# Kernel optimization log

Hardware: AMD Instinct MI355X
Metric: run time of the kernel (lower is better)

## Reference

```python
import jax, jax.numpy as jnp
import numpy as np

BS, D_IN, D_OUT, N_MASKS = 1024, 512, 512, 8

def setup_inputs() -> dict:
    key = jax.random.key(0)
    k1, k2, k3, k4 = jax.random.split(key, 4)
    x = jax.random.normal(k1, (BS, D_IN), dtype=jnp.float32)
    state = jax.random.randint(k2, (BS,), 0, N_MASKS, dtype=jnp.int32)
    # glorot-uniform-like kernel
    limit = float(np.sqrt(6.0 / (D_IN + D_OUT)))
    kernel = jax.random.uniform(k3, (D_IN, D_OUT), dtype=jnp.float32, minval=-limit, maxval=limit)
    # binary MADE connectivity masks (0/1)
    masks = (jax.random.uniform(k4, (N_MASKS, D_IN, D_OUT)) < 0.5).astype(jnp.float32)
    return {"x": x, "state": state, "kernel": kernel, "masks": masks}

def reference(x, state, kernel, masks):
    # Math of original: out = relu(x[b] @ (kernel * masks[state[b]]))
    # Efficient form: precompute all n masked kernels (small n), batched matmul,
    # then gather per-sample result. Avoids materializing [bs, d_in, d_out].
    masked = kernel[None, :, :] * masks            # [n, d_in, d_out]
    y_all = jnp.einsum('bi,nio->bno', x, masked)   # [bs, n, d_out]
    y = jnp.take_along_axis(y_all, state[:, None, None].astype(jnp.int32), axis=1)[:, 0, :]
    return jax.nn.relu(y)
```

## Files before the change

### kernel.cpp

```cpp
#include <hip/hip_runtime.h>

#define BS 1024
#define D_IN 512
#define D_OUT 512
#define N_MASKS 8

typedef short bf16x8 __attribute__((ext_vector_type(8)));
typedef float f32x4 __attribute__((ext_vector_type(4)));

#define WF_OFF_USH (8192 / 2)
#define WF_USH     (N_MASKS * 16 * 32 * 512)
#define XB_OFF_USH (WF_OFF_USH + WF_USH)

__device__ __forceinline__ ushort f2bf(float f) {
    union { float f; unsigned u; } x; x.f = f;
    unsigned r = (x.u + 0x7fffu + ((x.u >> 16) & 1u)) >> 16;
    return (ushort)r;
}

__global__ void __launch_bounds__(256) prep_kernel(
    const float* __restrict__ x, const int* __restrict__ state,
    const float* __restrict__ kern, const float* __restrict__ masks,
    int* __restrict__ wsi, ushort* __restrict__ wf, ushort* __restrict__ xb)
{
    __shared__ float prod[32][133];
    const int bx  = blockIdx.x;
    const int tid = threadIdx.x;

    if (bx < 512) {
        const int n  = bx >> 6;
        const int kb = (bx >> 2) & 15;
        const int cg = bx & 3;
        const int k0 = kb * 32, c0 = cg * 128;
        const float* maskn = masks + (size_t)n * (D_IN * D_OUT);

        #pragma unroll
        for (int it = 0; it < 4; ++it) {
            const int i  = it * 256 + tid;
            const int r  = i >> 5;
            const int c4 = i & 31;
            const size_t gidx = (size_t)(k0 + r) * D_OUT + c0 + c4 * 4;
            const float4 kv = *(const float4*)&kern[gidx];
            const float4 mv = *(const float4*)&maskn[gidx];
            float* dst = &prod[r][c4 * 4];
            dst[0] = kv.x * mv.x; dst[1] = kv.y * mv.y;
            dst[2] = kv.z * mv.z; dst[3] = kv.w * mv.w;
        }
        __syncthreads();

        #pragma unroll
        for (int it = 0; it < 2; ++it) {
            const int c = it * 64 + (tid >> 2);
            const int q = tid & 3;
            uint pk[4];
            #pragma unroll
            for (int h = 0; h < 4; ++h) {
                const float v0 = prod[q * 8 + 2 * h][c];
                const float v1 = prod[q * 8 + 2 * h + 1][c];
                pk[h] = (uint)f2bf(v0) | ((uint)f2bf(v1) << 16);
            }
            uint4 o; o.x = pk[0]; o.y = pk[1]; o.z = pk[2]; o.w = pk[3];
            const int cb = cg * 8 + (c >> 4);
            const int l  = q * 16 + (c & 15);
            *(uint4*)(wf + ((size_t)((n * 16 + kb) * 32 + cb)) * 512 + l * 8) = o;
        }
    } else if (bx < 768) {
        const int idx = (bx - 512) * 256 + tid;
        const float4 a = ((const float4*)x)[idx * 2];
        const float4 b = ((const float4*)x)[idx * 2 + 1];
        uint4 o;
        o.x = (uint)f2bf(a.x) | ((uint)f2bf(a.y) << 16);
        o.y = (uint)f2bf(a.z) | ((uint)f2bf(a.w) << 16);
        o.z = (uint)f2bf(b.x) | ((uint)f2bf(b.y) << 16);
        o.w = (uint)f2bf(b.z) | ((uint)f2bf(b.w) << 16);
        *(uint4*)(xb + (size_t)idx * 8) = o;
    } else {
        __shared__ int cnt[N_MASKS];
        __shared__ int offs[N_MASKS + 1];
        if (tid < N_MASKS) cnt[tid] = 0;
        __syncthreads();
        int s[4];
        #pragma unroll
        for (int r = 0; r < 4; ++r) {
            s[r] = state[r * 256 + tid];
            atomicAdd(&cnt[s[r]], 1);
        }
        __syncthreads();
        if (tid == 0) {
            int acc = 0;
            for (int i = 0; i < N_MASKS; ++i) { offs[i] = acc; acc += cnt[i]; }
            offs[N_MASKS] = acc;
        }
        __syncthreads();
        if (tid <= N_MASKS) wsi[tid] = offs[tid];
        if (tid < N_MASKS) cnt[tid] = offs[tid];
        __syncthreads();
        #pragma unroll
        for (int r = 0; r < 4; ++r) {
            const int pos = atomicAdd(&cnt[s[r]], 1);
            wsi[16 + pos] = r * 256 + tid;
        }
    }
}

__global__ void __launch_bounds__(256, 4) gemm_kernel(
    const ushort* __restrict__ xb, const ushort* __restrict__ wf,
    const int* __restrict__ wsi, float* __restrict__ out)
{
    const int n   = blockIdx.x;
    const int cb0 = blockIdx.y * 2;
    const int off0 = wsi[n];
    const int off1 = wsi[n + 1];
    const int gcnt = off1 - off0;

    const int tid  = threadIdx.x;
    const int lane = tid & 63;
    const int wid  = tid >> 6;
    const int g    = lane >> 4;
    const int cl   = lane & 15;

    __shared__ float red[3][2][64][4];

    const ushort* wp0 = wf + ((size_t)((n * 16 + wid * 4) * 32 + cb0)) * 512 + lane * 8;

    for (int rt = blockIdx.z; rt * 16 < gcnt; rt += 8) {
        const int p  = off0 + rt * 16 + cl;
        const int rv = (p < off1) ? wsi[16 + p] : -1;
        const ushort* xr = xb + (size_t)(rv < 0 ? 0 : rv) * D_IN + wid * 4 * 32 + g * 8;

        f32x4 acc0 = {0.f, 0.f, 0.f, 0.f};
        f32x4 acc1 = {0.f, 0.f, 0.f, 0.f};
        #pragma unroll
        for (int i = 0; i < 4; ++i) {
            const bf16x8 a  = *(const bf16x8*)(xr + i * 32);
            const bf16x8 b0 = *(const bf16x8*)(wp0 + (size_t)i * 32 * 512);
            const bf16x8 b1 = *(const bf16x8*)(wp0 + (size_t)i * 32 * 512 + 512);
            acc0 = __builtin_amdgcn_mfma_f32_16x16x32_bf16(a, b0, acc0, 0, 0, 0);
            acc1 = __builtin_amdgcn_mfma_f32_16x16x32_bf16(a, b1, acc1, 0, 0, 0);
        }

        if (wid) {
            *(f32x4*)&red[wid - 1][0][lane][0] = acc0;
            *(f32x4*)&red[wid - 1][1][lane][0] = acc1;
        }
        __syncthreads();
        if (wid == 0) {
            #pragma unroll
            for (int w = 0; w < 3; ++w) {
                acc0 += *(const f32x4*)&red[w][0][lane][0];
                acc1 += *(const f32x4*)&red[w][1][lane][0];
            }
            #pragma unroll
            for (int r = 0; r < 4; ++r) {
                const int brow = __shfl(rv, g * 4 + r);
                if (brow >= 0) {
                    float* op = out + (size_t)brow * D_OUT;
                    op[cb0 * 16 + cl]       = fmaxf(acc0[r], 0.f);
                    op[(cb0 + 1) * 16 + cl] = fmaxf(acc1[r], 0.f);
                }
            }
        }
        __syncthreads();
    }
}

extern "C" void kernel_launch(void* const* d_in, const int* in_sizes, int n_in,
                              void* d_out, int out_size, void* d_ws, size_t ws_size,
                              hipStream_t stream) {
    const float* x     = (const float*)d_in[0];
    const int*   state = (const int*)d_in[1];
    const float* kern  = (const float*)d_in[2];
    const float* masks = (const float*)d_in[3];
    float*  out = (float*)d_out;
    int*    wsi = (int*)d_ws;
    ushort* wsu = (ushort*)d_ws;

    prep_kernel<<<769, 256, 0, stream>>>(x, state, kern, masks,
                                         wsi, wsu + WF_OFF_USH, wsu + XB_OFF_USH);
    dim3 grid(N_MASKS, 16, 8);
    gemm_kernel<<<grid, 256, 0, stream>>>(wsu + XB_OFF_USH, wsu + WF_OFF_USH, wsi, out);
}
```

Measured before the change: 15.45 us.

## Fuse x bf16 conversion into GEMM and use fixed-slot per-mask row buckets

The separate prep pass that converts x to bf16 is removed; the GEMM now loads fp32 x rows directly and packs them to bf16 in registers. The prefix-sum bucketing of rows by mask is replaced by fixed 256-entry slots per mask, filled with -1 and then with row indices via shared-memory atomics. The GEMM grid covers every slot tile, and a tile exits early when it has no valid rows. This removes a launch phase's worth of blocks, the xb round trip and the per-block row-tile loop. In exchange the GEMM reads twice the x bytes, and any mask with more than 256 rows would silently drop rows.

```diff
diff --git a/kernel.cpp b/kernel.cpp
--- a/kernel.cpp
+++ b/kernel.cpp
@@ -4,13 +4,12 @@
 #define D_IN 512
 #define D_OUT 512
 #define N_MASKS 8
+#define SLOTS 256
 
 typedef short bf16x8 __attribute__((ext_vector_type(8)));
 typedef float f32x4 __attribute__((ext_vector_type(4)));
 
 #define WF_OFF_USH (8192 / 2)
-#define WF_USH     (N_MASKS * 16 * 32 * 512)
-#define XB_OFF_USH (WF_OFF_USH + WF_USH)
 
 __device__ __forceinline__ ushort f2bf(float f) {
     union { float f; unsigned u; } x; x.f = f;
@@ -18,10 +17,19 @@
     return (ushort)r;
 }
 
+__device__ __forceinline__ bf16x8 pack8(float4 a0, float4 a1) {
+    union { uint u[4]; bf16x8 v; } r;
+    r.u[0] = (uint)f2bf(a0.x) | ((uint)f2bf(a0.y) << 16);
+    r.u[1] = (uint)f2bf(a0.z) | ((uint)f2bf(a0.w) << 16);
+    r.u[2] = (uint)f2bf(a1.x) | ((uint)f2bf(a1.y) << 16);
+    r.u[3] = (uint)f2bf(a1.z) | ((uint)f2bf(a1.w) << 16);
+    return r.v;
+}
+
 __global__ void __launch_bounds__(256) prep_kernel(
-    const float* __restrict__ x, const int* __restrict__ state,
+    const int* __restrict__ state,
     const float* __restrict__ kern, const float* __restrict__ masks,
-    int* __restrict__ wsi, ushort* __restrict__ wf, ushort* __restrict__ xb)
+    int* __restrict__ perm, ushort* __restrict__ wf)
 {
     __shared__ float prod[32][133];
     const int bx  = blockIdx.x;
@@ -64,54 +72,30 @@
             const int l  = q * 16 + (c & 15);
             *(uint4*)(wf + ((size_t)((n * 16 + kb) * 32 + cb)) * 512 + l * 8) = o;
         }
-    } else if (bx < 768) {
-        const int idx = (bx - 512) * 256 + tid;
-        const float4 a = ((const float4*)x)[idx * 2];
-        const float4 b = ((const float4*)x)[idx * 2 + 1];
-        uint4 o;
-        o.x = (uint)f2bf(a.x) | ((uint)f2bf(a.y) << 16);
-        o.y = (uint)f2bf(a.z) | ((uint)f2bf(a.w) << 16);
-        o.z = (uint)f2bf(b.x) | ((uint)f2bf(b.y) << 16);
-        o.w = (uint)f2bf(b.z) | ((uint)f2bf(b.w) << 16);
-        *(uint4*)(xb + (size_t)idx * 8) = o;
     } else {
         __shared__ int cnt[N_MASKS];
-        __shared__ int offs[N_MASKS + 1];
         if (tid < N_MASKS) cnt[tid] = 0;
-        __syncthreads();
-        int s[4];
         #pragma unroll
-        for (int r = 0; r < 4; ++r) {
-            s[r] = state[r * 256 + tid];
-            atomicAdd(&cnt[s[r]], 1);
-        }
-        __syncthreads();
-        if (tid == 0) {
-            int acc = 0;
-            for (int i = 0; i < N_MASKS; ++i) { offs[i] = acc; acc += cnt[i]; }
-            offs[N_MASKS] = acc;
-        }
-        __syncthreads();
-        if (tid <= N_MASKS) wsi[tid] = offs[tid];
-        if (tid < N_MASKS) cnt[tid] = offs[tid];
+        for (int i = 0; i < (N_MASKS * SLOTS) / 256; ++i)
+            perm[i * 256 + tid] = -1;
         __syncthreads();
         #pragma unroll
         for (int r = 0; r < 4; ++r) {
-            const int pos = atomicAdd(&cnt[s[r]], 1);
-            wsi[16 + pos] = r * 256 + tid;
+            const int row = r * 256 + tid;
+            const int s   = state[row];
+            const int pos = atomicAdd(&cnt[s], 1);
+            if (pos < SLOTS) perm[s * SLOTS + pos] = row;
         }
     }
 }
 
 __global__ void __launch_bounds__(256, 4) gemm_kernel(
-    const ushort* __restrict__ xb, const ushort* __restrict__ wf,
-    const int* __restrict__ wsi, float* __restrict__ out)
+    const float* __restrict__ x, const ushort* __restrict__ wf,
+    const int* __restrict__ perm, float* __restrict__ out)
 {
     const int n   = blockIdx.x;
     const int cb0 = blockIdx.y * 2;
-    const int off0 = wsi[n];
-    const int off1 = wsi[n + 1];
-    const int gcnt = off1 - off0;
+    const int rt  = blockIdx.z;
 
     const int tid  = threadIdx.x;
     const int lane = tid & 63;
@@ -119,48 +103,47 @@
     const int g    = lane >> 4;
     const int cl   = lane & 15;
 
+    const int rv = perm[n * SLOTS + rt * 16 + cl];
+    if (__ballot(rv >= 0) == 0ull) return;
+
     __shared__ float red[3][2][64][4];
 
     const ushort* wp0 = wf + ((size_t)((n * 16 + wid * 4) * 32 + cb0)) * 512 + lane * 8;
+    const float*  xr  = x + (size_t)(rv < 0 ? 0 : rv) * D_IN + wid * 128 + g * 8;
 
-    for (int rt = blockIdx.z; rt * 16 < gcnt; rt += 8) {
-        const int p  = off0 + rt * 16 + cl;
-        const int rv = (p < off1) ? wsi[16 + p] : -1;
-        const ushort* xr = xb + (size_t)(rv < 0 ? 0 : rv) * D_IN + wid * 4 * 32 + g * 8;
+    f32x4 acc0 = {0.f, 0.f, 0.f, 0.f};
+    f32x4 acc1 = {0.f, 0.f, 0.f, 0.f};
+    #pragma unroll
+    for (int i = 0; i < 4; ++i) {
+        const float4 a0 = *(const float4*)(xr + i * 32);
+        const float4 a1 = *(const float4*)(xr + i * 32 + 4);
+        const bf16x8 a  = pack8(a0, a1);
+        const bf16x8 b0 = *(const bf16x8*)(wp0 + (size_t)i * 32 * 512);
+        const bf16x8 b1 = *(const bf16x8*)(wp0 + (size_t)i * 32 * 512 + 512);
+        acc0 = __builtin_amdgcn_mfma_f32_16x16x32_bf16(a, b0, acc0, 0, 0, 0);
+        acc1 = __builtin_amdgcn_mfma_f32_16x16x32_bf16(a, b1, acc1, 0, 0, 0);
+    }
 
-        f32x4 acc0 = {0.f, 0.f, 0.f, 0.f};
-        f32x4 acc1 = {0.f, 0.f, 0.f, 0.f};
+    if (wid) {
+        *(f32x4*)&red[wid - 1][0][lane][0] = acc0;
+        *(f32x4*)&red[wid - 1][1][lane][0] = acc1;
+    }
+    __syncthreads();
+    if (wid == 0) {
         #pragma unroll
-        for (int i = 0; i < 4; ++i) {
-            const bf16x8 a  = *(const bf16x8*)(xr + i * 32);
-            const bf16x8 b0 = *(const bf16x8*)(wp0 + (size_t)i * 32 * 512);
-            const bf16x8 b1 = *(const bf16x8*)(wp0 + (size_t)i * 32 * 512 + 512);
-            acc0 = __builtin_amdgcn_mfma_f32_16x16x32_bf16(a, b0, acc0, 0, 0, 0);
-            acc1 = __builtin_amdgcn_mfma_f32_16x16x32_bf16(a, b1, acc1, 0, 0, 0);
+        for (int w = 0; w < 3; ++w) {
+            acc0 += *(const f32x4*)&red[w][0][lane][0];
+            acc1 += *(const f32x4*)&red[w][1][lane][0];
         }
-
-        if (wid) {
-            *(f32x4*)&red[wid - 1][0][lane][0] = acc0;
-            *(f32x4*)&red[wid - 1][1][lane][0] = acc1;
-        }
-        __syncthreads();
-        if (wid == 0) {
-            #pragma unroll
-            for (int w = 0; w < 3; ++w) {
-                acc0 += *(const f32x4*)&red[w][0][lane][0];
-                acc1 += *(const f32x4*)&red[w][1][lane][0];
-            }
-            #pragma unroll
-            for (int r = 0; r < 4; ++r) {
-                const int brow = __shfl(rv, g * 4 + r);
-                if (brow >= 0) {
-                    float* op = out + (size_t)brow * D_OUT;
-                    op[cb0 * 16 + cl]       = fmaxf(acc0[r], 0.f);
-                    op[(cb0 + 1) * 16 + cl] = fmaxf(acc1[r], 0.f);
-                }
+        #pragma unroll
+        for (int r = 0; r < 4; ++r) {
+            const int brow = __shfl(rv, g * 4 + r);
+            if (brow >= 0) {
+                float* op = out + (size_t)brow * D_OUT;
+                op[cb0 * 16 + cl]       = fmaxf(acc0[r], 0.f);
+                op[(cb0 + 1) * 16 + cl] = fmaxf(acc1[r], 0.f);
             }
         }
-        __syncthreads();
     }
 }
 
@@ -171,12 +154,11 @@
     const int*   state = (const int*)d_in[1];
     const float* kern  = (const float*)d_in[2];
     const float* masks = (const float*)d_in[3];
-    float*  out = (float*)d_out;
-    int*    wsi = (int*)d_ws;
-    ushort* wsu = (ushort*)d_ws;
+    float*  out  = (float*)d_out;
+    int*    perm = (int*)d_ws;
+    ushort* wsu  = (ushort*)d_ws;
 
-    prep_kernel<<<769, 256, 0, stream>>>(x, state, kern, masks,
-                                         wsi, wsu + WF_OFF_USH, wsu + XB_OFF_USH);
-    dim3 grid(N_MASKS, 16, 8);
-    gemm_kernel<<<grid, 256, 0, stream>>>(wsu + XB_OFF_USH, wsu + WF_OFF_USH, wsi, out);
+    prep_kernel<<<513, 256, 0, stream>>>(state, kern, masks, perm, wsu + WF_OFF_USH);
+    dim3 grid(N_MASKS, 16, SLOTS / 16);
+    gemm_kernel<<<grid, 256, 0, stream>>>(x, wsu + WF_OFF_USH, perm, out);
 }
```

New measurement: 17.82 us. 1.15x slower.
